# Performance work log

Measured on AMD Instinct MI355X. Metric: run time of the kernel, lower is better.

Reference implementation:

```python
import jax, jax.numpy as jnp
import numpy as np

N_NODES = 20000
N_EDGES = 320000
IN_CH = 256
HID_CH = 256   # 2 * out_channels
OUT_CH = 128


def gcn_conv(x, edge_index, W, b, n_nodes):
    """PyG GCNConv: linear transform, add self-loops, sym-normalized scatter-add."""
    x = x @ W  # [N, C_out]
    loop = jnp.arange(n_nodes, dtype=edge_index.dtype)
    row = jnp.concatenate([edge_index[0], loop])  # source nodes
    col = jnp.concatenate([edge_index[1], loop])  # destination nodes
    deg = jax.ops.segment_sum(jnp.ones_like(col, dtype=x.dtype), col,
                              num_segments=n_nodes)
    deg_inv_sqrt = jnp.where(deg > 0, jax.lax.rsqrt(deg), 0.0)
    norm = deg_inv_sqrt[row] * deg_inv_sqrt[col]  # [E+N]
    msg = x[row] * norm[:, None]                  # gather + scale
    out = jax.ops.segment_sum(msg, col, num_segments=n_nodes)  # scatter-add
    return out + b


def setup_inputs() -> dict:
    key = jax.random.key(0)
    k1, k2, k3, k4, k5 = jax.random.split(key, 5)
    doc_embeds = jax.random.normal(k1, (N_NODES, IN_CH), dtype=jnp.float32)
    edge_index = jax.random.randint(k2, (2, N_EDGES), 0, N_NODES, dtype=jnp.int64)
    # Glorot-style init for GCN weights, zero bias (PyG defaults)
    s1 = 1.0 / np.sqrt(IN_CH)
    s2 = 1.0 / np.sqrt(HID_CH)
    W1 = jax.random.uniform(k3, (IN_CH, HID_CH), jnp.float32, -s1, s1)
    b1 = jnp.zeros((HID_CH,), jnp.float32)
    W2 = jax.random.uniform(k4, (HID_CH, OUT_CH), jnp.float32, -s2, s2)
    b2 = jnp.zeros((OUT_CH,), jnp.float32)
    return {"doc_embeds": doc_embeds, "edge_index": edge_index,
            "W1": W1, "b1": b1, "W2": W2, "b2": b2}


def reference(doc_embeds, edge_index, W1, b1, W2, b2):
    n = doc_embeds.shape[0]
    x = jax.nn.relu(gcn_conv(doc_embeds, edge_index, W1, b1, n))
    x = gcn_conv(x, edge_index, W2, b2, n)
    return x
```

## Files before the change

kernel.cpp:

```cpp
#include <hip/hip_runtime.h>
#include <math.h>

#define N_NODES 20000
#define N_EDGES 320000
#define IN_CH   256
#define HID_CH  256
#define OUT_CH  128
#define CAP     64
#define GK      256

typedef __attribute__((ext_vector_type(8))) short short8;
typedef __attribute__((ext_vector_type(8))) unsigned short ushort8;
typedef __attribute__((ext_vector_type(4))) unsigned short ushort4v;
typedef __attribute__((ext_vector_type(4))) float floatx4;
typedef __attribute__((ext_vector_type(2))) float floatx2;
typedef __attribute__((ext_vector_type(2))) _Float16 half2v;
typedef __attribute__((ext_vector_type(8))) _Float16 half8;

static __device__ __forceinline__ unsigned short f2bf(float f) {
    unsigned int u = __float_as_uint(f);
    u += 0x7FFFu + ((u >> 16) & 1u);
    return (unsigned short)(u >> 16);
}
static __device__ __forceinline__ float bf2f(unsigned short h) {
    return __uint_as_float(((unsigned int)h) << 16);
}

__global__ __launch_bounds__(256)
void prep_kernel(const float* __restrict__ W1, const float* __restrict__ W2,
                 unsigned short* __restrict__ W1thi, unsigned short* __restrict__ W1tlo,
                 unsigned short* __restrict__ W2thi, unsigned short* __restrict__ W2tlo,
                 const int* __restrict__ row, const int* __restrict__ col,
                 int* __restrict__ deg, unsigned short* __restrict__ srcs) {
    const int g = blockIdx.x * blockDim.x + threadIdx.x;
    const int gsz = gridDim.x * blockDim.x;
    for (int t = g; t < (IN_CH * HID_CH) / 16; t += gsz) {
        int n = t >> 4;
        int kc = (t & 15) * 16;
        ushort8 h0, l0, h1, l1;
#pragma unroll
        for (int j = 0; j < 8; ++j) {
            float x = W1[(size_t)(kc + j) * HID_CH + n];
            h0[j] = f2bf(x); l0[j] = f2bf(x - bf2f(h0[j]));
            float y = W1[(size_t)(kc + 8 + j) * HID_CH + n];
            h1[j] = f2bf(y); l1[j] = f2bf(y - bf2f(h1[j]));
        }
        *(ushort8*)(W1thi + (size_t)n * IN_CH + kc)     = h0;
        *(ushort8*)(W1thi + (size_t)n * IN_CH + kc + 8) = h1;
        *(ushort8*)(W1tlo + (size_t)n * IN_CH + kc)     = l0;
        *(ushort8*)(W1tlo + (size_t)n * IN_CH + kc + 8) = l1;
    }
    for (int t = g; t < (HID_CH * OUT_CH) / 16; t += gsz) {
        int n = t >> 4;
        int kc = (t & 15) * 16;
        ushort8 h0, l0, h1, l1;
#pragma unroll
        for (int j = 0; j < 8; ++j) {
            float x = W2[(size_t)(kc + j) * OUT_CH + n];
            h0[j] = f2bf(x); l0[j] = f2bf(x - bf2f(h0[j]));
            float y = W2[(size_t)(kc + 8 + j) * OUT_CH + n];
            h1[j] = f2bf(y); l1[j] = f2bf(y - bf2f(h1[j]));
        }
        *(ushort8*)(W2thi + (size_t)n * HID_CH + kc)     = h0;
        *(ushort8*)(W2thi + (size_t)n * HID_CH + kc + 8) = h1;
        *(ushort8*)(W2tlo + (size_t)n * HID_CH + kc)     = l0;
        *(ushort8*)(W2tlo + (size_t)n * HID_CH + kc + 8) = l1;
    }
    for (int i = g; i < N_EDGES; i += gsz) {
        int c = col[i];
        int r = row[i];
        int p = atomicAdd(&deg[c], 1);
        srcs[(size_t)c * CAP + p] = (unsigned short)r;
    }
}

template <int AMODE, int TN>
__global__ __launch_bounds__(256, 2)
void gemm_mfma_kernel(const float* __restrict__ Afp, const _Float16* __restrict__ Ah,
                      const unsigned short* __restrict__ Bthi, const unsigned short* __restrict__ Btlo,
                      const int* __restrict__ deg, _Float16* __restrict__ C, int M, int N) {
    constexpr int NJ = TN / 32;
    __shared__ unsigned short As[2][64][36];
    __shared__ unsigned short Bs[2][TN][36];
    const int tid = threadIdx.x;
    const int m0 = blockIdx.y * 64;
    const int lane = tid & 63;
    const int wave = tid >> 6;
    const int wr = (wave >> 1) * 32;
    const int wc = (wave & 1) * (TN / 2);
    const int lm = lane & 15;
    const int lk = (lane >> 4) * 8;

    floatx4 acc[2][NJ];
#pragma unroll
    for (int i = 0; i < 2; ++i)
#pragma unroll
        for (int j = 0; j < NJ; ++j) acc[i][j] = (floatx4){0.f, 0.f, 0.f, 0.f};

    const int ar  = tid >> 2;
    const int ako = (tid & 3) * 8;

    for (int k0 = 0; k0 < GK; k0 += 32) {
        {
            ushort8 vh = {}, vl = {};
            if (m0 + ar < M) {
                float xs[8];
                if (AMODE == 1) {
                    const float* ap = Afp + (size_t)(m0 + ar) * GK + k0 + ako;
                    float4 f0 = *(const float4*)ap;
                    float4 f1 = *(const float4*)(ap + 4);
                    xs[0] = f0.x; xs[1] = f0.y; xs[2] = f0.z; xs[3] = f0.w;
                    xs[4] = f1.x; xs[5] = f1.y; xs[6] = f1.z; xs[7] = f1.w;
                } else {
                    half8 hv = *(const half8*)(Ah + (size_t)(m0 + ar) * GK + k0 + ako);
#pragma unroll
                    for (int j = 0; j < 8; ++j) xs[j] = (float)hv[j];
                }
#pragma unroll
                for (int j = 0; j < 8; ++j) {
                    vh[j] = f2bf(xs[j]);
                    vl[j] = f2bf(xs[j] - bf2f(vh[j]));
                }
            }
            *(ushort8*)&As[0][ar][ako] = vh;
            *(ushort8*)&As[1][ar][ako] = vl;
        }
#pragma unroll
        for (int c = 0; c < TN / 64; ++c) {
            int ch = tid + c * 256;
            int r  = ch >> 2;
            int ko = (ch & 3) * 8;
            size_t gb = (size_t)r * GK + k0 + ko;
            *(ushort8*)&Bs[0][r][ko] = *(const ushort8*)(Bthi + gb);
            *(ushort8*)&Bs[1][r][ko] = *(const ushort8*)(Btlo + gb);
        }
        __syncthreads();

        short8 ah[2], al[2];
#pragma unroll
        for (int i = 0; i < 2; ++i) {
            ah[i] = *(const short8*)&As[0][wr + i * 16 + lm][lk];
            al[i] = *(const short8*)&As[1][wr + i * 16 + lm][lk];
        }
#pragma unroll
        for (int j = 0; j < NJ; ++j) {
            short8 bh = *(const short8*)&Bs[0][wc + j * 16 + lm][lk];
            short8 bl = *(const short8*)&Bs[1][wc + j * 16 + lm][lk];
#pragma unroll
            for (int i = 0; i < 2; ++i) {
                acc[i][j] = __builtin_amdgcn_mfma_f32_16x16x32_bf16(ah[i], bh, acc[i][j], 0, 0, 0);
                acc[i][j] = __builtin_amdgcn_mfma_f32_16x16x32_bf16(ah[i], bl, acc[i][j], 0, 0, 0);
                acc[i][j] = __builtin_amdgcn_mfma_f32_16x16x32_bf16(al[i], bh, acc[i][j], 0, 0, 0);
            }
        }
        __syncthreads();
    }

#pragma unroll
    for (int i = 0; i < 2; ++i) {
#pragma unroll
        for (int r = 0; r < 4; ++r) {
            int rowi = m0 + wr + i * 16 + (lane >> 4) * 4 + r;
            if (rowi < M) {
                float dr = 1.0f / sqrtf((float)(deg[rowi] + 1));
#pragma unroll
                for (int j = 0; j < NJ; ++j) {
                    C[(size_t)rowi * N + wc + j * 16 + lm] = (_Float16)(dr * acc[i][j][r]);
                }
            }
        }
    }
}

template <int C, int NSLICE, int MODE>
__global__ __launch_bounds__(256)
void gather_sliced_kernel(const _Float16* __restrict__ X, const int* __restrict__ deg,
                          const unsigned short* __restrict__ srcs,
                          const float* __restrict__ bias, float* __restrict__ outf,
                          _Float16* __restrict__ outh, int n) {
    constexpr int SW = C / NSLICE;
    static_assert(SW == 32, "slice must be 32 channels");
    const int slice = blockIdx.x % NSLICE;
    const int ngrp  = blockIdx.x / NSLICE;
    const int wave = threadIdx.x >> 6;
    const int lane = threadIdx.x & 63;
    const int g  = lane >> 4;
    const int sl = lane & 15;
    const int node = ngrp * 16 + wave * 4 + g;
    if (node >= n) return;
    const int choff = slice * SW + sl * 2;
    const size_t beg = (size_t)node * CAP;
    const int cnt = deg[node];

    float a0 = 0.f, a1 = 0.f;
    int e = 0;
    for (; e + 4 <= cnt; e += 4) {
        ushort4v s4 = *(const ushort4v*)(srcs + beg + e);
        half2v v0 = *(const half2v*)(X + (size_t)s4.x * C + choff);
        half2v v1 = *(const half2v*)(X + (size_t)s4.y * C + choff);
        half2v v2 = *(const half2v*)(X + (size_t)s4.z * C + choff);
        half2v v3 = *(const half2v*)(X + (size_t)s4.w * C + choff);
        a0 += (float)v0.x + (float)v1.x + (float)v2.x + (float)v3.x;
        a1 += (float)v0.y + (float)v1.y + (float)v2.y + (float)v3.y;
    }
    for (; e < cnt; ++e) {
        int r = srcs[beg + e];
        half2v v = *(const half2v*)(X + (size_t)r * C + choff);
        a0 += (float)v.x; a1 += (float)v.y;
    }

    const float dc = 1.0f / sqrtf((float)(cnt + 1));
    half2v vsh = *(const half2v*)(X + (size_t)node * C + choff);
    float2 bb = *(const float2*)(bias + choff);

    float o0 = dc * (a0 + (float)vsh.x) + bb.x;
    float o1 = dc * (a1 + (float)vsh.y) + bb.y;

    if constexpr (MODE == 1) {
        half2v h;
        h.x = (_Float16)fmaxf(o0, 0.f);
        h.y = (_Float16)fmaxf(o1, 0.f);
        *(half2v*)(outh + (size_t)node * C + choff) = h;
    } else {
        floatx2 o = {o0, o1};
        __builtin_nontemporal_store(o, (floatx2*)(outf + (size_t)node * C + choff));
    }
}

extern "C" void kernel_launch(void* const* d_in, const int* in_sizes, int n_in,
                              void* d_out, int out_size, void* d_ws, size_t ws_size,
                              hipStream_t stream) {
    const float* doc_embeds = (const float*)d_in[0];
    const int*   edge_index = (const int*)d_in[1];
    const float* W1 = (const float*)d_in[2];
    const float* b1 = (const float*)d_in[3];
    const float* W2 = (const float*)d_in[4];
    const float* b2 = (const float*)d_in[5];
    float* out = (float*)d_out;

    const int* row = edge_index;
    const int* col = edge_index + N_EDGES;

    char* ws = (char*)d_ws;
    auto align_up = [](size_t x) { return (x + 255) / 256 * 256; };

    _Float16* X1s = (_Float16*)(ws);
    _Float16* H1  = (_Float16*)(ws + align_up((size_t)N_NODES * HID_CH * 2));
    _Float16* X2s = X1s;
    char* meta = (char*)(ws + 2 * align_up((size_t)N_NODES * HID_CH * 2));
    unsigned short* W1thi = (unsigned short*)(meta); meta += align_up((size_t)IN_CH * HID_CH * 2);
    unsigned short* W1tlo = (unsigned short*)(meta); meta += align_up((size_t)IN_CH * HID_CH * 2);
    unsigned short* W2thi = (unsigned short*)(meta); meta += align_up((size_t)HID_CH * OUT_CH * 2);
    unsigned short* W2tlo = (unsigned short*)(meta); meta += align_up((size_t)HID_CH * OUT_CH * 2);
    int*            deg   = (int*)(meta);            meta += align_up((size_t)N_NODES * 4);
    unsigned short* srcs  = (unsigned short*)(meta);

    hipMemsetAsync(deg, 0, (size_t)N_NODES * 4, stream);
    prep_kernel<<<(N_EDGES + 255) / 256, 256, 0, stream>>>(
        W1, W2, W1thi, W1tlo, W2thi, W2tlo, row, col, deg, srcs);

    {
        dim3 grid(1, (N_NODES + 63) / 64);
        gemm_mfma_kernel<1, 256><<<grid, 256, 0, stream>>>(
            doc_embeds, nullptr, W1thi, W1tlo, deg, X1s, N_NODES, HID_CH);
    }
    gather_sliced_kernel<HID_CH, 8, 1><<<((N_NODES + 15) / 16) * 8, 256, 0, stream>>>(
        X1s, deg, srcs, b1, nullptr, H1, N_NODES);

    {
        dim3 grid(1, (N_NODES + 63) / 64);
        gemm_mfma_kernel<2, 128><<<grid, 256, 0, stream>>>(
            nullptr, H1, W2thi, W2tlo, deg, X2s, N_NODES, OUT_CH);
    }
    gather_sliced_kernel<OUT_CH, 4, 0><<<((N_NODES + 15) / 16) * 4, 256, 0, stream>>>(
        X2s, deg, srcs, b2, out, nullptr, N_NODES);
}
```

Before: 179.7 us.

## Replace split-bf16 three-pass MFMA with single fp16 MFMA and tile GEMM1 over N

Drops the hi/lo bf16 split emulation of fp32 (three MFMAs per tile, two LDS copies of A and B) in favour of a single fp16 MFMA on fp16-converted inputs and weights. The weight prep writes one fp16 transposed copy instead of two bf16 copies. The first GEMM is split into two 128-column tiles along N for more blocks. This cuts MFMA count, LDS traffic and conversion work, at the cost of fp16 precision on the input embeddings and weights.

```diff
diff --git a/kernel.cpp b/kernel.cpp
--- a/kernel.cpp
+++ b/kernel.cpp
@@ -17,19 +17,9 @@
 typedef __attribute__((ext_vector_type(2))) _Float16 half2v;
 typedef __attribute__((ext_vector_type(8))) _Float16 half8;
 
-static __device__ __forceinline__ unsigned short f2bf(float f) {
-    unsigned int u = __float_as_uint(f);
-    u += 0x7FFFu + ((u >> 16) & 1u);
-    return (unsigned short)(u >> 16);
-}
-static __device__ __forceinline__ float bf2f(unsigned short h) {
-    return __uint_as_float(((unsigned int)h) << 16);
-}
-
 __global__ __launch_bounds__(256)
 void prep_kernel(const float* __restrict__ W1, const float* __restrict__ W2,
-                 unsigned short* __restrict__ W1thi, unsigned short* __restrict__ W1tlo,
-                 unsigned short* __restrict__ W2thi, unsigned short* __restrict__ W2tlo,
+                 _Float16* __restrict__ W1t, _Float16* __restrict__ W2t,
                  const int* __restrict__ row, const int* __restrict__ col,
                  int* __restrict__ deg, unsigned short* __restrict__ srcs) {
     const int g = blockIdx.x * blockDim.x + threadIdx.x;
@@ -37,34 +27,26 @@
     for (int t = g; t < (IN_CH * HID_CH) / 16; t += gsz) {
         int n = t >> 4;
         int kc = (t & 15) * 16;
-        ushort8 h0, l0, h1, l1;
+        half8 h0, h1;
 #pragma unroll
         for (int j = 0; j < 8; ++j) {
-            float x = W1[(size_t)(kc + j) * HID_CH + n];
-            h0[j] = f2bf(x); l0[j] = f2bf(x - bf2f(h0[j]));
-            float y = W1[(size_t)(kc + 8 + j) * HID_CH + n];
-            h1[j] = f2bf(y); l1[j] = f2bf(y - bf2f(h1[j]));
-        }
-        *(ushort8*)(W1thi + (size_t)n * IN_CH + kc)     = h0;
-        *(ushort8*)(W1thi + (size_t)n * IN_CH + kc + 8) = h1;
-        *(ushort8*)(W1tlo + (size_t)n * IN_CH + kc)     = l0;
-        *(ushort8*)(W1tlo + (size_t)n * IN_CH + kc + 8) = l1;
+            h0[j] = (_Float16)W1[(size_t)(kc + j) * HID_CH + n];
+            h1[j] = (_Float16)W1[(size_t)(kc + 8 + j) * HID_CH + n];
+        }
+        *(half8*)(W1t + (size_t)n * IN_CH + kc)     = h0;
+        *(half8*)(W1t + (size_t)n * IN_CH + kc + 8) = h1;
     }
     for (int t = g; t < (HID_CH * OUT_CH) / 16; t += gsz) {
         int n = t >> 4;
         int kc = (t & 15) * 16;
-        ushort8 h0, l0, h1, l1;
+        half8 h0, h1;
 #pragma unroll
         for (int j = 0; j < 8; ++j) {
-            float x = W2[(size_t)(kc + j) * OUT_CH + n];
-            h0[j] = f2bf(x); l0[j] = f2bf(x - bf2f(h0[j]));
-            float y = W2[(size_t)(kc + 8 + j) * OUT_CH + n];
-            h1[j] = f2bf(y); l1[j] = f2bf(y - bf2f(h1[j]));
-        }
-        *(ushort8*)(W2thi + (size_t)n * HID_CH + kc)     = h0;
-        *(ushort8*)(W2thi + (size_t)n * HID_CH + kc + 8) = h1;
-        *(ushort8*)(W2tlo + (size_t)n * HID_CH + kc)     = l0;
-        *(ushort8*)(W2tlo + (size_t)n * HID_CH + kc + 8) = l1;
+            h0[j] = (_Float16)W2[(size_t)(kc + j) * OUT_CH + n];
+            h1[j] = (_Float16)W2[(size_t)(kc + 8 + j) * OUT_CH + n];
+        }
+        *(half8*)(W2t + (size_t)n * HID_CH + kc)     = h0;
+        *(half8*)(W2t + (size_t)n * HID_CH + kc + 8) = h1;
     }
     for (int i = g; i < N_EDGES; i += gsz) {
         int c = col[i];
@@ -77,13 +59,14 @@
 template <int AMODE, int TN>
 __global__ __launch_bounds__(256, 2)
 void gemm_mfma_kernel(const float* __restrict__ Afp, const _Float16* __restrict__ Ah,
-                      const unsigned short* __restrict__ Bthi, const unsigned short* __restrict__ Btlo,
+                      const _Float16* __restrict__ Bt,
                       const int* __restrict__ deg, _Float16* __restrict__ C, int M, int N) {
     constexpr int NJ = TN / 32;
-    __shared__ unsigned short As[2][64][36];
-    __shared__ unsigned short Bs[2][TN][36];
+    __shared__ _Float16 As[64][36];
+    __shared__ _Float16 Bs[TN][36];
     const int tid = threadIdx.x;
     const int m0 = blockIdx.y * 64;
+    const int n0 = blockIdx.x * TN;
     const int lane = tid & 63;
     const int wave = tid >> 6;
     const int wr = (wave >> 1) * 32;
@@ -102,56 +85,41 @@
 
     for (int k0 = 0; k0 < GK; k0 += 32) {
         {
-            ushort8 vh = {}, vl = {};
+            half8 va = {};
             if (m0 + ar < M) {
-                float xs[8];
                 if (AMODE == 1) {
                     const float* ap = Afp + (size_t)(m0 + ar) * GK + k0 + ako;
                     float4 f0 = *(const float4*)ap;
                     float4 f1 = *(const float4*)(ap + 4);
-                    xs[0] = f0.x; xs[1] = f0.y; xs[2] = f0.z; xs[3] = f0.w;
-                    xs[4] = f1.x; xs[5] = f1.y; xs[6] = f1.z; xs[7] = f1.w;
+                    va[0] = (_Float16)f0.x; va[1] = (_Float16)f0.y;
+                    va[2] = (_Float16)f0.z; va[3] = (_Float16)f0.w;
+                    va[4] = (_Float16)f1.x; va[5] = (_Float16)f1.y;
+                    va[6] = (_Float16)f1.z; va[7] = (_Float16)f1.w;
                 } else {
-                    half8 hv = *(const half8*)(Ah + (size_t)(m0 + ar) * GK + k0 + ako);
-#pragma unroll
-                    for (int j = 0; j < 8; ++j) xs[j] = (float)hv[j];
-                }
-#pragma unroll
-                for (int j = 0; j < 8; ++j) {
-                    vh[j] = f2bf(xs[j]);
-                    vl[j] = f2bf(xs[j] - bf2f(vh[j]));
+                    va = *(const half8*)(Ah + (size_t)(m0 + ar) * GK + k0 + ako);
                 }
             }
-            *(ushort8*)&As[0][ar][ako] = vh;
-            *(ushort8*)&As[1][ar][ako] = vl;
+            *(half8*)&As[ar][ako] = va;
         }
 #pragma unroll
         for (int c = 0; c < TN / 64; ++c) {
             int ch = tid + c * 256;
             int r  = ch >> 2;
             int ko = (ch & 3) * 8;
-            size_t gb = (size_t)r * GK + k0 + ko;
-            *(ushort8*)&Bs[0][r][ko] = *(const ushort8*)(Bthi + gb);
-            *(ushort8*)&Bs[1][r][ko] = *(const ushort8*)(Btlo + gb);
+            *(half8*)&Bs[r][ko] = *(const half8*)(Bt + (size_t)(n0 + r) * GK + k0 + ko);
         }
         __syncthreads();
 
-        short8 ah[2], al[2];
-#pragma unroll
-        for (int i = 0; i < 2; ++i) {
-            ah[i] = *(const short8*)&As[0][wr + i * 16 + lm][lk];
-            al[i] = *(const short8*)&As[1][wr + i * 16 + lm][lk];
-        }
+        half8 ah[2];
+#pragma unroll
+        for (int i = 0; i < 2; ++i)
+            ah[i] = *(const half8*)&As[wr + i * 16 + lm][lk];
 #pragma unroll
         for (int j = 0; j < NJ; ++j) {
-            short8 bh = *(const short8*)&Bs[0][wc + j * 16 + lm][lk];
-            short8 bl = *(const short8*)&Bs[1][wc + j * 16 + lm][lk];
-#pragma unroll
-            for (int i = 0; i < 2; ++i) {
-                acc[i][j] = __builtin_amdgcn_mfma_f32_16x16x32_bf16(ah[i], bh, acc[i][j], 0, 0, 0);
-                acc[i][j] = __builtin_amdgcn_mfma_f32_16x16x32_bf16(ah[i], bl, acc[i][j], 0, 0, 0);
-                acc[i][j] = __builtin_amdgcn_mfma_f32_16x16x32_bf16(al[i], bh, acc[i][j], 0, 0, 0);
-            }
+            half8 bh = *(const half8*)&Bs[wc + j * 16 + lm][lk];
+#pragma unroll
+            for (int i = 0; i < 2; ++i)
+                acc[i][j] = __builtin_amdgcn_mfma_f32_16x16x32_f16(ah[i], bh, acc[i][j], 0, 0, 0);
         }
         __syncthreads();
     }
@@ -165,7 +133,7 @@
                 float dr = 1.0f / sqrtf((float)(deg[rowi] + 1));
 #pragma unroll
                 for (int j = 0; j < NJ; ++j) {
-                    C[(size_t)rowi * N + wc + j * 16 + lm] = (_Float16)(dr * acc[i][j][r]);
+                    C[(size_t)rowi * N + n0 + wc + j * 16 + lm] = (_Float16)(dr * acc[i][j][r]);
                 }
             }
         }
@@ -248,29 +216,27 @@
     _Float16* H1  = (_Float16*)(ws + align_up((size_t)N_NODES * HID_CH * 2));
     _Float16* X2s = X1s;
     char* meta = (char*)(ws + 2 * align_up((size_t)N_NODES * HID_CH * 2));
-    unsigned short* W1thi = (unsigned short*)(meta); meta += align_up((size_t)IN_CH * HID_CH * 2);
-    unsigned short* W1tlo = (unsigned short*)(meta); meta += align_up((size_t)IN_CH * HID_CH * 2);
-    unsigned short* W2thi = (unsigned short*)(meta); meta += align_up((size_t)HID_CH * OUT_CH * 2);
-    unsigned short* W2tlo = (unsigned short*)(meta); meta += align_up((size_t)HID_CH * OUT_CH * 2);
-    int*            deg   = (int*)(meta);            meta += align_up((size_t)N_NODES * 4);
-    unsigned short* srcs  = (unsigned short*)(meta);
+    _Float16* W1t = (_Float16*)(meta); meta += align_up((size_t)IN_CH * HID_CH * 2);
+    _Float16* W2t = (_Float16*)(meta); meta += align_up((size_t)HID_CH * OUT_CH * 2);
+    int*            deg  = (int*)(meta);            meta += align_up((size_t)N_NODES * 4);
+    unsigned short* srcs = (unsigned short*)(meta);
 
     hipMemsetAsync(deg, 0, (size_t)N_NODES * 4, stream);
     prep_kernel<<<(N_EDGES + 255) / 256, 256, 0, stream>>>(
-        W1, W2, W1thi, W1tlo, W2thi, W2tlo, row, col, deg, srcs);
+        W1, W2, W1t, W2t, row, col, deg, srcs);
 
     {
-        dim3 grid(1, (N_NODES + 63) / 64);
-        gemm_mfma_kernel<1, 256><<<grid, 256, 0, stream>>>(
-            doc_embeds, nullptr, W1thi, W1tlo, deg, X1s, N_NODES, HID_CH);
+        dim3 grid(HID_CH / 128, (N_NODES + 63) / 64);
+        gemm_mfma_kernel<1, 128><<<grid, 256, 0, stream>>>(
+            doc_embeds, nullptr, W1t, deg, X1s, N_NODES, HID_CH);
     }
     gather_sliced_kernel<HID_CH, 8, 1><<<((N_NODES + 15) / 16) * 8, 256, 0, stream>>>(
         X1s, deg, srcs, b1, nullptr, H1, N_NODES);
 
     {
-        dim3 grid(1, (N_NODES + 63) / 64);
+        dim3 grid(OUT_CH / 128, (N_NODES + 63) / 64);
         gemm_mfma_kernel<2, 128><<<grid, 256, 0, stream>>>(
-            nullptr, H1, W2thi, W2tlo, deg, X2s, N_NODES, OUT_CH);
+            nullptr, H1, W2t, deg, X2s, N_NODES, OUT_CH);
     }
     gather_sliced_kernel<OUT_CH, 4, 0><<<((N_NODES + 15) / 16) * 4, 256, 0, stream>>>(
         X2s, deg, srcs, b2, out, nullptr, N_NODES);
```

After: 166.0 us. 1.08x faster.
